# Performance work log

Measured on AMD Instinct MI355X. Metric: run time of the kernel, lower is better.

Reference implementation:

```python
import jax, jax.numpy as jnp
import numpy as np

NA, NM, NT = 4353, 3676, 8000
N = NA + NM + NT
E = 500000
S = 200000
D_IN, DP, DE, DC, HID = 512, 256, 128, 64, 16


def setup_inputs() -> dict:
    key = jax.random.key(0)
    ks = jax.random.split(key, 32)
    f = lambda k, shp, s: (jax.random.normal(k, shp, jnp.float32) * s)
    inp = {
        'h_author': f(ks[0], (NA, D_IN), 1.0),
        'h_movie': f(ks[1], (NM, D_IN), 1.0),
        'h_term': f(ks[2], (NT, D_IN), 1.0),
        'Wp_author': f(ks[3], (D_IN, DP), D_IN ** -0.5),
        'Wp_movie': f(ks[4], (D_IN, DP), D_IN ** -0.5),
        'Wp_term': f(ks[5], (D_IN, DP), D_IN ** -0.5),
        'W1': f(ks[6], (DP, DE), DP ** -0.5),
        'b1': jnp.zeros((DE,), jnp.float32),
        'W2': f(ks[7], (DE, DE), DE ** -0.5),
        'b2': jnp.zeros((DE,), jnp.float32),
        'Wc_author': f(ks[8], (DE, DC), DE ** -0.5),
        'Wc_movie': f(ks[9], (DE, DC), DE ** -0.5),
        'Wc_term': f(ks[10], (DE, DC), DE ** -0.5),
        'Wh_author': f(ks[11], (DE + 2 * DC, HID), (DE + 2 * DC) ** -0.5),
        'Wh_movie': f(ks[12], (DE + 2 * DC, HID), (DE + 2 * DC) ** -0.5),
        'Wh_term': f(ks[13], (DE + 2 * DC, HID), (DE + 2 * DC) ** -0.5),
        'Wo_author': f(ks[14], (HID, 1), HID ** -0.5),
        'Wo_movie': f(ks[15], (HID, 1), HID ** -0.5),
        'Wo_term': f(ks[16], (HID, 1), HID ** -0.5),
        'src': jax.random.randint(ks[17], (E,), 0, N),
        'dst': jax.random.randint(ks[18], (E,), 0, N),
        'ns0_author': jax.random.randint(ks[19], (S,), 0, NA),
        'ns0_movie': jax.random.randint(ks[20], (S,), 0, NM),
        'ns0_term': jax.random.randint(ks[21], (S,), 0, NT),
        'ns1_author': jax.random.randint(ks[22], (S,), 0, NA),
        'ns1_movie': jax.random.randint(ks[23], (S,), 0, NM),
        'ns1_term': jax.random.randint(ks[24], (S,), 0, NT),
        'ns2_author': jax.random.randint(ks[25], (S,), 0, NA),
        'ns2_movie': jax.random.randint(ks[26], (S,), 0, NM),
        'ns2_term': jax.random.randint(ks[27], (S,), 0, NT),
    }
    return inp


def reference(h_author, h_movie, h_term, Wp_author, Wp_movie, Wp_term,
              W1, b1, W2, b2, Wc_author, Wc_movie, Wc_term,
              Wh_author, Wh_movie, Wh_term, Wo_author, Wo_movie, Wo_term,
              src, dst, ns0_author, ns0_movie, ns0_term,
              ns1_author, ns1_movie, ns1_term, ns2_author, ns2_movie, ns2_term):
    # per-ntype feature projection (bias=False), concat in ntype order -> homogeneous [N, DP]
    H = jnp.concatenate([h_author @ Wp_author, h_movie @ Wp_movie, h_term @ Wp_term], axis=0)
    # GraphConv(norm='none'): out = (sum over in-edges of src feat) @ W + b
    agg1 = jax.ops.segment_sum(H[src], dst, num_segments=N)      # [N, DP]
    h1 = jax.nn.relu(agg1 @ W1 + b1)                             # [N, DE]
    agg2 = jax.ops.segment_sum(h1[src], dst, num_segments=N)    # [N, DE]
    h2 = agg2 @ W2 + b2
    # F.normalize(p=2, dim=1, eps=1e-12)
    h = h2 / jnp.maximum(jnp.linalg.norm(h2, axis=1, keepdims=True), 1e-12)
    ha, hm, ht = h[:NA], h[NA:NA + NM], h[NA + NM:]
    # per-ntype context encoder (bias=False)
    ca, cm, ct = ha @ Wc_author, hm @ Wc_movie, ht @ Wc_term

    def cls(feat, Wh, Wo):
        return jax.nn.relu(feat @ Wh) @ Wo  # multi_2Linear, bias=False

    # target emb first, then context of other ntypes in ntype order
    t0 = jnp.concatenate([ha[ns0_author], cm[ns0_movie], ct[ns0_term]], axis=1)
    t1 = jnp.concatenate([hm[ns1_movie], ca[ns1_author], ct[ns1_term]], axis=1)
    t2 = jnp.concatenate([ht[ns2_term], ca[ns2_author], cm[ns2_movie]], axis=1)
    p = jnp.concatenate([cls(t0, Wh_author, Wo_author),
                         cls(t1, Wh_movie, Wo_movie),
                         cls(t2, Wh_term, Wo_term)], axis=0)
    x = jax.nn.sigmoid(p).ravel()
    out_h_movie = h[4353:8029]
    return h, x, out_h_movie
```

## Files before the change

kernel.cpp:

```cpp
#include <hip/hip_runtime.h>
#include <hip/hip_bf16.h>

namespace {
constexpr int kNA = 4353, kNM = 3676, kNT = 8000;
constexpr int kN  = kNA + kNM + kNT;
constexpr int kE  = 500000;
constexpr int kS  = 200000;
constexpr int kDIN = 512, kDP = 256, kDE = 128, kDC = 64;

constexpr size_t OUT_X  = (size_t)kN * kDE;
constexpr size_t OUT_HM = OUT_X + 3ull * kS;

constexpr size_t align256(size_t x) { return (x + 255) & ~size_t(255); }

constexpr size_t OFF_WPW1 = 0;
constexpr size_t OFF_M9   = OFF_WPW1 + 3ull * 512 * 128 * 4;
constexpr size_t OFF_HW1  = align256(OFF_M9 + 9ull * 2048 * 4);
constexpr size_t OFF_H1   = OFF_HW1 + (size_t)kN * kDE * 4;
constexpr size_t OFF_AGG2 = OFF_H1  + (size_t)kN * kDE * 4;
constexpr size_t OFF_HN   = OFF_AGG2 + (size_t)kN * kDE * 4;
constexpr size_t OFF_P    = OFF_HN  + (size_t)kN * kDE * 4;
constexpr size_t OFF_ESRC = align256(OFF_P + 3ull * kN * 16 * 4);
constexpr size_t OFF_RP   = align256(OFF_ESRC + (size_t)kE * 4);
constexpr size_t OFF_CUR  = align256(OFF_RP + (size_t)(kN + 1) * 4);
constexpr size_t WS_NEEDED = align256(OFF_CUR + (size_t)kN * 4);

constexpr int kBA = (kNA + 15) / 16;
constexpr int kBM = (kNM + 15) / 16;
constexpr int kBT = (kNT + 15) / 16;
constexpr int kHW1Blocks = kBA + kBM + kBT;
constexpr int kG2Blocks  = (kN + 15) / 16;
}

__global__ __launch_bounds__(128) void prep1_kernel(
    const float* __restrict__ WpA, const float* __restrict__ WpM,
    const float* __restrict__ WpT, const float* __restrict__ W1,
    float* __restrict__ WpW1)
{
    int b = blockIdx.x;
    int t = b >> 7;
    int k0 = (b & 127) * 4;
    const float* Wp = (t == 0) ? WpA : ((t == 1) ? WpM : WpT);
    int c = threadIdx.x;
    float acc[4] = {0.f, 0.f, 0.f, 0.f};
    for (int j = 0; j < kDP; j++) {
        float w1 = W1[j * kDE + c];
#pragma unroll
        for (int r = 0; r < 4; r++)
            acc[r] += Wp[(k0 + r) * kDP + j] * w1;
    }
#pragma unroll
    for (int r = 0; r < 4; r++)
        WpW1[((size_t)t * kDIN + k0 + r) * kDE + c] = acc[r];
}

__global__ __launch_bounds__(256) void prep2_kernel(
    const float* __restrict__ WhA, const float* __restrict__ WhM,
    const float* __restrict__ WhT,
    const float* __restrict__ WcA, const float* __restrict__ WcM,
    const float* __restrict__ WcT,
    float* __restrict__ M9)
{
    int b = blockIdx.x;
    int g = b / 3, t = b % 3;
    const float* Wh = (g == 0) ? WhA : ((g == 1) ? WhM : WhT);
    const float* Wc = (t == 0) ? WcA : ((t == 1) ? WcM : WcT);
    int slot;
    if (t == g) slot = 0;
    else {
        int lower = (g == 0) ? 1 : 0;
        slot = (t == lower) ? 128 : 192;
    }
    float* Mout = M9 + (size_t)b * 2048;
    for (int idx = threadIdx.x; idx < 2048; idx += 256) {
        int k = idx >> 4, j = idx & 15;
        float v;
        if (slot == 0) v = Wh[k * 16 + j];
        else {
            v = 0.f;
            for (int d = 0; d < kDC; d++)
                v += Wc[k * kDC + d] * Wh[(slot + d) * 16 + j];
        }
        Mout[idx] = v;
    }
}

__global__ __launch_bounds__(256) void hw1_kernel(
    const float* __restrict__ hA, const float* __restrict__ hM,
    const float* __restrict__ hT, const float* __restrict__ WpW1,
    float* __restrict__ HW1)
{
    __shared__ float AL[16 * kDIN];
    int b = blockIdx.x;
    const float *A, *W; int typeN, rowBase, lb;
    if (b < kBA)             { lb = b;             A = hA; W = WpW1;                   typeN = kNA; rowBase = 0; }
    else if (b < kBA + kBM)  { lb = b - kBA;       A = hM; W = WpW1 + 1ull*kDIN*kDE;   typeN = kNM; rowBase = kNA; }
    else                     { lb = b - kBA - kBM; A = hT; W = WpW1 + 2ull*kDIN*kDE;   typeN = kNT; rowBase = kNA + kNM; }
    int r0 = lb * 16;

    const float4* Ag = (const float4*)A;
#pragma unroll
    for (int i = 0; i < 8; i++) {
        int f = threadIdx.x + i * 256;
        int rl = f >> 7, k4 = f & 127;
        int gr = min(r0 + rl, typeN - 1);
        ((float4*)AL)[f] = Ag[(size_t)gr * 128 + k4];
    }
    __syncthreads();

    int col = threadIdx.x & 127;
    int hh  = threadIdx.x >> 7;
    const float* ALh = AL + hh * 8 * kDIN;
    float acc[8];
#pragma unroll
    for (int r = 0; r < 8; r++) acc[r] = 0.f;

    for (int k0 = 0; k0 < kDIN; k0 += 8) {
        float w[8];
#pragma unroll
        for (int i = 0; i < 8; i++)
            w[i] = W[(size_t)(k0 + i) * kDE + col];
#pragma unroll
        for (int r = 0; r < 8; r++) {
            const float4 a0 = *(const float4*)(ALh + r * kDIN + k0);
            const float4 a1 = *(const float4*)(ALh + r * kDIN + k0 + 4);
            acc[r] += a0.x * w[0] + a0.y * w[1] + a0.z * w[2] + a0.w * w[3]
                    + a1.x * w[4] + a1.y * w[5] + a1.z * w[6] + a1.w * w[7];
        }
    }
#pragma unroll
    for (int r = 0; r < 8; r++) {
        int lr = r0 + hh * 8 + r;
        if (lr < typeN) HW1[(size_t)(rowBase + lr) * kDE + col] = acc[r];
    }
}

__device__ __forceinline__ int clampN(int v) { return min(max(v, 0), kN - 1); }

__global__ __launch_bounds__(256) void hist_kernel(const int* __restrict__ key,
                                                   int* __restrict__ counts)
{
    int e = blockIdx.x * 256 + threadIdx.x;
    if (e < kE) atomicAdd(&counts[clampN(key[e])], 1);
}

__global__ __launch_bounds__(256) void scan_kernel(int* __restrict__ cnt_cur,
                                                   int* __restrict__ rowptr)
{
    __shared__ int sums[256];
    int tid = threadIdx.x;
    int i0 = tid * 63, i1 = min(i0 + 63, kN);
    int s = 0;
    for (int i = i0; i < i1; i++) s += cnt_cur[i];
    sums[tid] = s;
    __syncthreads();
    if (tid == 0) {
        int run = 0;
        for (int i = 0; i < 256; i++) { int v = sums[i]; sums[i] = run; run += v; }
    }
    __syncthreads();
    int base = sums[tid];
    for (int i = i0; i < i1; i++) {
        int c = cnt_cur[i];
        rowptr[i] = base;
        cnt_cur[i] = base;
        base += c;
    }
    if (tid == 0) rowptr[kN] = kE;
}

__global__ __launch_bounds__(256) void fill_kernel(const int* __restrict__ stored,
                                                   const int* __restrict__ key,
                                                   int* __restrict__ cursor,
                                                   int* __restrict__ esrc)
{
    int e = blockIdx.x * 256 + threadIdx.x;
    if (e < kE) {
        int p = atomicAdd(&cursor[clampN(key[e])], 1);
        esrc[min(p, kE - 1)] = clampN(stored[e]);
    }
}

__global__ __launch_bounds__(kDE) void agg_relu_kernel(const float* __restrict__ X,
                                                       const int* __restrict__ rowptr,
                                                       const int* __restrict__ esrc,
                                                       const float* __restrict__ b1,
                                                       float* __restrict__ out)
{
    int n = blockIdx.x, tid = threadIdx.x;
    int j = rowptr[n], end = rowptr[n + 1];
    float a0 = 0.f, a1 = 0.f, a2 = 0.f, a3 = 0.f;
    for (; j + 3 < end; j += 4) {
        int s0 = esrc[j], s1 = esrc[j + 1], s2 = esrc[j + 2], s3 = esrc[j + 3];
        a0 += X[(size_t)s0 * kDE + tid];
        a1 += X[(size_t)s1 * kDE + tid];
        a2 += X[(size_t)s2 * kDE + tid];
        a3 += X[(size_t)s3 * kDE + tid];
    }
    for (; j < end; j++) a0 += X[(size_t)esrc[j] * kDE + tid];
    out[(size_t)n * kDE + tid] = fmaxf((a0 + a1) + (a2 + a3) + b1[tid], 0.f);
}

__global__ __launch_bounds__(kDE) void agg_kernel(const float* __restrict__ X,
                                                  const int* __restrict__ rowptr,
                                                  const int* __restrict__ esrc,
                                                  float* __restrict__ out)
{
    int n = blockIdx.x, tid = threadIdx.x;
    int j = rowptr[n], end = rowptr[n + 1];
    float a0 = 0.f, a1 = 0.f, a2 = 0.f, a3 = 0.f;
    for (; j + 3 < end; j += 4) {
        int s0 = esrc[j], s1 = esrc[j + 1], s2 = esrc[j + 2], s3 = esrc[j + 3];
        a0 += X[(size_t)s0 * kDE + tid];
        a1 += X[(size_t)s1 * kDE + tid];
        a2 += X[(size_t)s2 * kDE + tid];
        a3 += X[(size_t)s3 * kDE + tid];
    }
    for (; j < end; j++) a0 += X[(size_t)esrc[j] * kDE + tid];
    out[(size_t)n * kDE + tid] = (a0 + a1) + (a2 + a3);
}

__global__ __launch_bounds__(256) void gemm2_norm_kernel(
    const float* __restrict__ X, const float* __restrict__ W2,
    const float* __restrict__ b2, float* __restrict__ hn,
    float* __restrict__ out)
{
    __shared__ float AL[16 * kDE];
    __shared__ float red[16][2];
    int r0 = blockIdx.x * 16;

    const float4* Xg = (const float4*)X;
#pragma unroll
    for (int i = 0; i < 2; i++) {
        int f = threadIdx.x + i * 256;
        int rl = f >> 5, k4 = f & 31;
        int gr = min(r0 + rl, kN - 1);
        ((float4*)AL)[f] = Xg[(size_t)gr * 32 + k4];
    }
    __syncthreads();

    int col = threadIdx.x & 127;
    int hh  = threadIdx.x >> 7;
    const float* ALh = AL + hh * 8 * kDE;
    float acc[8];
#pragma unroll
    for (int r = 0; r < 8; r++) acc[r] = 0.f;

    for (int k0 = 0; k0 < kDE; k0 += 8) {
        float w[8];
#pragma unroll
        for (int i = 0; i < 8; i++)
            w[i] = W2[(size_t)(k0 + i) * kDE + col];
#pragma unroll
        for (int r = 0; r < 8; r++) {
            const float4 a0 = *(const float4*)(ALh + r * kDE + k0);
            const float4 a1 = *(const float4*)(ALh + r * kDE + k0 + 4);
            acc[r] += a0.x * w[0] + a0.y * w[1] + a0.z * w[2] + a0.w * w[3]
                    + a1.x * w[4] + a1.y * w[5] + a1.z * w[6] + a1.w * w[7];
        }
    }

    float bv = b2[col];
    int half = (threadIdx.x >> 6) & 1;
#pragma unroll
    for (int r = 0; r < 8; r++) {
        float v = acc[r] + bv;
        acc[r] = v;
        float ss = v * v;
#pragma unroll
        for (int o = 32; o > 0; o >>= 1) ss += __shfl_xor(ss, o);
        if ((threadIdx.x & 63) == 0) red[hh * 8 + r][half] = ss;
    }
    __syncthreads();
#pragma unroll
    for (int r = 0; r < 8; r++) {
        int gr = r0 + hh * 8 + r;
        if (gr < kN) {
            float tot = red[hh * 8 + r][0] + red[hh * 8 + r][1];
            float sc = 1.f / fmaxf(sqrtf(tot), 1e-12f);
            float hv = acc[r] * sc;
            hn[(size_t)gr * kDE + col] = hv;
            out[(size_t)gr * kDE + col] = hv;
            if (gr >= kNA && gr < kNA + kNM)
                out[OUT_HM + (size_t)(gr - kNA) * kDE + col] = hv;
        }
    }
}

__global__ __launch_bounds__(128) void partial_kernel(const float* __restrict__ hn,
                                                      const float* __restrict__ M9,
                                                      float* __restrict__ P)
{
    int b = blockIdx.x;
    int g = b / 2005, b2 = b % 2005;
    int t, lb, typeN, rowBase;
    if (b2 < 545)       { t = 0; lb = b2;        typeN = kNA; rowBase = 0; }
    else if (b2 < 1005) { t = 1; lb = b2 - 545;  typeN = kNM; rowBase = kNA; }
    else                { t = 2; lb = b2 - 1005; typeN = kNT; rowBase = kNA + kNM; }
    const float* M = M9 + (size_t)(g * 3 + t) * 2048;
    int r = threadIdx.x >> 4, j = threadIdx.x & 15;
    int lr = lb * 8 + r;
    if (lr >= typeN) return;
    int n = rowBase + lr;
    float acc = 0.f;
    for (int k = 0; k < kDE; k += 4) {
        const float4 h4 = *(const float4*)(hn + (size_t)n * kDE + k);
        acc += h4.x * M[(k + 0) * 16 + j] + h4.y * M[(k + 1) * 16 + j]
             + h4.z * M[(k + 2) * 16 + j] + h4.w * M[(k + 3) * 16 + j];
    }
    P[((size_t)g * kN + n) * 16 + j] = acc;
}

__global__ __launch_bounds__(256) void cls_lite_kernel(
    const float* __restrict__ P,
    const int* __restrict__ n0a, const int* __restrict__ n0m, const int* __restrict__ n0t,
    const int* __restrict__ n1a, const int* __restrict__ n1m, const int* __restrict__ n1t,
    const int* __restrict__ n2a, const int* __restrict__ n2m, const int* __restrict__ n2t,
    const float* __restrict__ WoA, const float* __restrict__ WoM, const float* __restrict__ WoT,
    float* __restrict__ out, int blocksPerGroup)
{
    int g = blockIdx.x / blocksPerGroup;
    int i = (blockIdx.x % blocksPerGroup) * 256 + threadIdx.x;
    if (i >= kS) return;
    auto cA = [](int v){ return min(max(v, 0), kNA - 1); };
    auto cM = [](int v){ return min(max(v, 0), kNM - 1); };
    auto cT = [](int v){ return min(max(v, 0), kNT - 1); };
    int ra, rb, rc;
    if (g == 0)      { ra = cA(n0a[i]);             rb = kNA + cM(n0m[i]);  rc = kNA + kNM + cT(n0t[i]); }
    else if (g == 1) { ra = kNA + cM(n1m[i]);       rb = cA(n1a[i]);        rc = kNA + kNM + cT(n1t[i]); }
    else             { ra = kNA + kNM + cT(n2t[i]); rb = cA(n2a[i]);        rc = kNA + cM(n2m[i]); }
    const float* Pg = P + (size_t)g * kN * 16;
    const float* wo = (g == 0) ? WoA : ((g == 1) ? WoM : WoT);
    const float4* pa = (const float4*)(Pg + (size_t)ra * 16);
    const float4* pb = (const float4*)(Pg + (size_t)rb * 16);
    const float4* pc = (const float4*)(Pg + (size_t)rc * 16);
    float p = 0.f;
#pragma unroll
    for (int q = 0; q < 4; q++) {
        float4 a = pa[q], b = pb[q], c = pc[q];
        p += fmaxf(a.x + b.x + c.x, 0.f) * wo[q * 4 + 0];
        p += fmaxf(a.y + b.y + c.y, 0.f) * wo[q * 4 + 1];
        p += fmaxf(a.z + b.z + c.z, 0.f) * wo[q * 4 + 2];
        p += fmaxf(a.w + b.w + c.w, 0.f) * wo[q * 4 + 3];
    }
    out[OUT_X + (size_t)g * kS + i] = 1.f / (1.f + expf(-p));
}

extern "C" void kernel_launch(void* const* d_in, const int* in_sizes, int n_in,
                              void* d_out, int out_size, void* d_ws, size_t ws_size,
                              hipStream_t stream)
{
    (void)out_size;
    static const int expected[30] = {
        2228736, 1882112, 4096000, 131072, 131072, 131072, 32768, 128, 16384, 128,
        8192, 8192, 8192, 4096, 4096, 4096, 16, 16, 16,
        500000, 500000, 200000, 200000, 200000, 200000, 200000, 200000, 200000, 200000, 200000 };
    if (n_in != 30) return;
    for (int i = 0; i < 30; i++) if (in_sizes[i] != expected[i]) return;
    if (ws_size < WS_NEEDED) return;

    const float* h_a  = (const float*)d_in[0];
    const float* h_m  = (const float*)d_in[1];
    const float* h_t  = (const float*)d_in[2];
    const float* Wp_a = (const float*)d_in[3];
    const float* Wp_m = (const float*)d_in[4];
    const float* Wp_t = (const float*)d_in[5];
    const float* W1   = (const float*)d_in[6];
    const float* b1   = (const float*)d_in[7];
    const float* W2   = (const float*)d_in[8];
    const float* b2   = (const float*)d_in[9];
    const float* Wc_a = (const float*)d_in[10];
    const float* Wc_m = (const float*)d_in[11];
    const float* Wc_t = (const float*)d_in[12];
    const float* Wh_a = (const float*)d_in[13];
    const float* Wh_m = (const float*)d_in[14];
    const float* Wh_t = (const float*)d_in[15];
    const float* Wo_a = (const float*)d_in[16];
    const float* Wo_m = (const float*)d_in[17];
    const float* Wo_t = (const float*)d_in[18];
    const int* src = (const int*)d_in[19];
    const int* dst = (const int*)d_in[20];

    char* ws = (char*)d_ws;
    float* WpW1  = (float*)(ws + OFF_WPW1);
    float* M9    = (float*)(ws + OFF_M9);
    float* HW1   = (float*)(ws + OFF_HW1);
    float* h1    = (float*)(ws + OFF_H1);
    float* agg2  = (float*)(ws + OFF_AGG2);
    float* hn    = (float*)(ws + OFF_HN);
    float* P     = (float*)(ws + OFF_P);
    int* esrc    = (int*)(ws + OFF_ESRC);
    int* rowptr  = (int*)(ws + OFF_RP);
    int* cursor  = (int*)(ws + OFF_CUR);
    float* out   = (float*)d_out;

    hipMemsetAsync(cursor, 0, (size_t)kN * 4, stream);

    hist_kernel<<<dim3(1954), dim3(256), 0, stream>>>(dst, cursor);
    scan_kernel<<<dim3(1), dim3(256), 0, stream>>>(cursor, rowptr);
    fill_kernel<<<dim3(1954), dim3(256), 0, stream>>>(src, dst, cursor, esrc);

    prep1_kernel<<<dim3(384), dim3(128), 0, stream>>>(Wp_a, Wp_m, Wp_t, W1, WpW1);
    prep2_kernel<<<dim3(9), dim3(256), 0, stream>>>(Wh_a, Wh_m, Wh_t, Wc_a, Wc_m, Wc_t, M9);

    hw1_kernel<<<dim3(kHW1Blocks), dim3(256), 0, stream>>>(h_a, h_m, h_t, WpW1, HW1);
    agg_relu_kernel<<<dim3(kN), dim3(kDE), 0, stream>>>(HW1, rowptr, esrc, b1, h1);
    agg_kernel<<<dim3(kN), dim3(kDE), 0, stream>>>(h1, rowptr, esrc, agg2);
    gemm2_norm_kernel<<<dim3(kG2Blocks), dim3(256), 0, stream>>>(agg2, W2, b2, hn, out);
    partial_kernel<<<dim3(6015), dim3(128), 0, stream>>>(hn, M9, P);
    cls_lite_kernel<<<dim3(2346), dim3(256), 0, stream>>>(P,
        (const int*)d_in[21], (const int*)d_in[22], (const int*)d_in[23],
        (const int*)d_in[24], (const int*)d_in[25], (const int*)d_in[26],
        (const int*)d_in[27], (const int*)d_in[28], (const int*)d_in[29],
        Wo_a, Wo_m, Wo_t, out, 782);
}
```

Baseline: 296.7 us.

## Register-tile hw1 GEMM with float4 and parallelize edge aggregation across warps

```diff
diff --git a/kernel.cpp b/kernel.cpp
--- a/kernel.cpp
+++ b/kernel.cpp
@@ -30,6 +30,7 @@
 constexpr int kBT = (kNT + 15) / 16;
 constexpr int kHW1Blocks = kBA + kBM + kBT;
 constexpr int kG2Blocks  = (kN + 15) / 16;
+constexpr int kAPad = kDIN + 4;
 }
 
 __global__ __launch_bounds__(128) void prep1_kernel(
@@ -90,7 +91,7 @@
     const float* __restrict__ hT, const float* __restrict__ WpW1,
     float* __restrict__ HW1)
 {
-    __shared__ float AL[16 * kDIN];
+    __shared__ float AL[16 * kAPad];
     int b = blockIdx.x;
     const float *A, *W; int typeN, rowBase, lb;
     if (b < kBA)             { lb = b;             A = hA; W = WpW1;                   typeN = kNA; rowBase = 0; }
@@ -104,35 +105,43 @@
         int f = threadIdx.x + i * 256;
         int rl = f >> 7, k4 = f & 127;
         int gr = min(r0 + rl, typeN - 1);
-        ((float4*)AL)[f] = Ag[(size_t)gr * 128 + k4];
-    }
-    __syncthreads();
-
-    int col = threadIdx.x & 127;
-    int hh  = threadIdx.x >> 7;
-    const float* ALh = AL + hh * 8 * kDIN;
-    float acc[8];
-#pragma unroll
-    for (int r = 0; r < 8; r++) acc[r] = 0.f;
-
-    for (int k0 = 0; k0 < kDIN; k0 += 8) {
-        float w[8];
-#pragma unroll
-        for (int i = 0; i < 8; i++)
-            w[i] = W[(size_t)(k0 + i) * kDE + col];
-#pragma unroll
-        for (int r = 0; r < 8; r++) {
-            const float4 a0 = *(const float4*)(ALh + r * kDIN + k0);
-            const float4 a1 = *(const float4*)(ALh + r * kDIN + k0 + 4);
-            acc[r] += a0.x * w[0] + a0.y * w[1] + a0.z * w[2] + a0.w * w[3]
-                    + a1.x * w[4] + a1.y * w[5] + a1.z * w[6] + a1.w * w[7];
-        }
-    }
-#pragma unroll
-    for (int r = 0; r < 8; r++) {
-        int lr = r0 + hh * 8 + r;
-        if (lr < typeN) HW1[(size_t)(rowBase + lr) * kDE + col] = acc[r];
-    }
+        *(float4*)(AL + rl * kAPad + k4 * 4) = Ag[(size_t)gr * 128 + k4];
+    }
+    __syncthreads();
+
+    int wave = threadIdx.x >> 6, lane = threadIdx.x & 63;
+    int cg = wave * 8 + (lane & 7);
+    int rg = lane >> 3;
+    int colbase = cg * 4;
+    const float* AL0 = AL + (2 * rg) * kAPad;
+    const float* AL1 = AL + (2 * rg + 1) * kAPad;
+
+    float4 acc0 = {0.f, 0.f, 0.f, 0.f};
+    float4 acc1 = {0.f, 0.f, 0.f, 0.f};
+
+#pragma unroll 2
+    for (int k0 = 0; k0 < kDIN; k0 += 4) {
+        const float4 w0 = *(const float4*)(W + (size_t)(k0 + 0) * kDE + colbase);
+        const float4 w1 = *(const float4*)(W + (size_t)(k0 + 1) * kDE + colbase);
+        const float4 w2 = *(const float4*)(W + (size_t)(k0 + 2) * kDE + colbase);
+        const float4 w3 = *(const float4*)(W + (size_t)(k0 + 3) * kDE + colbase);
+        const float4 a0 = *(const float4*)(AL0 + k0);
+        const float4 a1 = *(const float4*)(AL1 + k0);
+        acc0.x += a0.x * w0.x + a0.y * w1.x + a0.z * w2.x + a0.w * w3.x;
+        acc0.y += a0.x * w0.y + a0.y * w1.y + a0.z * w2.y + a0.w * w3.y;
+        acc0.z += a0.x * w0.z + a0.y * w1.z + a0.z * w2.z + a0.w * w3.z;
+        acc0.w += a0.x * w0.w + a0.y * w1.w + a0.z * w2.w + a0.w * w3.w;
+        acc1.x += a1.x * w0.x + a1.y * w1.x + a1.z * w2.x + a1.w * w3.x;
+        acc1.y += a1.x * w0.y + a1.y * w1.y + a1.z * w2.y + a1.w * w3.y;
+        acc1.z += a1.x * w0.z + a1.y * w1.z + a1.z * w2.z + a1.w * w3.z;
+        acc1.w += a1.x * w0.w + a1.y * w1.w + a1.z * w2.w + a1.w * w3.w;
+    }
+
+    int lr0 = r0 + 2 * rg, lr1 = lr0 + 1;
+    if (lr0 < typeN)
+        *(float4*)(HW1 + (size_t)(rowBase + lr0) * kDE + colbase) = acc0;
+    if (lr1 < typeN)
+        *(float4*)(HW1 + (size_t)(rowBase + lr1) * kDE + colbase) = acc1;
 }
 
 __device__ __forceinline__ int clampN(int v) { return min(max(v, 0), kN - 1); }
@@ -181,43 +190,45 @@
     }
 }
 
-__global__ __launch_bounds__(kDE) void agg_relu_kernel(const float* __restrict__ X,
-                                                       const int* __restrict__ rowptr,
-                                                       const int* __restrict__ esrc,
-                                                       const float* __restrict__ b1,
-                                                       float* __restrict__ out)
-{
-    int n = blockIdx.x, tid = threadIdx.x;
-    int j = rowptr[n], end = rowptr[n + 1];
-    float a0 = 0.f, a1 = 0.f, a2 = 0.f, a3 = 0.f;
-    for (; j + 3 < end; j += 4) {
-        int s0 = esrc[j], s1 = esrc[j + 1], s2 = esrc[j + 2], s3 = esrc[j + 3];
-        a0 += X[(size_t)s0 * kDE + tid];
-        a1 += X[(size_t)s1 * kDE + tid];
-        a2 += X[(size_t)s2 * kDE + tid];
-        a3 += X[(size_t)s3 * kDE + tid];
-    }
-    for (; j < end; j++) a0 += X[(size_t)esrc[j] * kDE + tid];
-    out[(size_t)n * kDE + tid] = fmaxf((a0 + a1) + (a2 + a3) + b1[tid], 0.f);
-}
-
-__global__ __launch_bounds__(kDE) void agg_kernel(const float* __restrict__ X,
-                                                  const int* __restrict__ rowptr,
-                                                  const int* __restrict__ esrc,
-                                                  float* __restrict__ out)
-{
-    int n = blockIdx.x, tid = threadIdx.x;
-    int j = rowptr[n], end = rowptr[n + 1];
-    float a0 = 0.f, a1 = 0.f, a2 = 0.f, a3 = 0.f;
-    for (; j + 3 < end; j += 4) {
-        int s0 = esrc[j], s1 = esrc[j + 1], s2 = esrc[j + 2], s3 = esrc[j + 3];
-        a0 += X[(size_t)s0 * kDE + tid];
-        a1 += X[(size_t)s1 * kDE + tid];
-        a2 += X[(size_t)s2 * kDE + tid];
-        a3 += X[(size_t)s3 * kDE + tid];
-    }
-    for (; j < end; j++) a0 += X[(size_t)esrc[j] * kDE + tid];
-    out[(size_t)n * kDE + tid] = (a0 + a1) + (a2 + a3);
+template <bool RELU>
+__global__ __launch_bounds__(256) void agg4_kernel(const float* __restrict__ X,
+                                                   const int* __restrict__ rowptr,
+                                                   const int* __restrict__ esrc,
+                                                   const float* __restrict__ b1,
+                                                   float* __restrict__ out)
+{
+    __shared__ float4 sh[8][32];
+    int n = blockIdx.x;
+    int eo = threadIdx.x >> 5;
+    int cg = threadIdx.x & 31;
+    int start = rowptr[n], end = rowptr[n + 1];
+    const float4* X4 = (const float4*)X;
+    float4 acc = {0.f, 0.f, 0.f, 0.f};
+    for (int j = start + eo; j < end; j += 8) {
+        int s = esrc[j];
+        float4 v = X4[(size_t)s * 32 + cg];
+        acc.x += v.x; acc.y += v.y; acc.z += v.z; acc.w += v.w;
+    }
+    sh[eo][cg] = acc;
+    __syncthreads();
+    if (threadIdx.x < 32) {
+        int c = threadIdx.x;
+        float4 s0 = sh[0][c], s1 = sh[1][c], s2 = sh[2][c], s3 = sh[3][c];
+        float4 s4 = sh[4][c], s5 = sh[5][c], s6 = sh[6][c], s7 = sh[7][c];
+        float4 r;
+        r.x = ((s0.x + s1.x) + (s2.x + s3.x)) + ((s4.x + s5.x) + (s6.x + s7.x));
+        r.y = ((s0.y + s1.y) + (s2.y + s3.y)) + ((s4.y + s5.y) + (s6.y + s7.y));
+        r.z = ((s0.z + s1.z) + (s2.z + s3.z)) + ((s4.z + s5.z) + (s6.z + s7.z));
+        r.w = ((s0.w + s1.w) + (s2.w + s3.w)) + ((s4.w + s5.w) + (s6.w + s7.w));
+        if (RELU) {
+            const float4 bv = ((const float4*)b1)[c];
+            r.x = fmaxf(r.x + bv.x, 0.f);
+            r.y = fmaxf(r.y + bv.y, 0.f);
+            r.z = fmaxf(r.z + bv.z, 0.f);
+            r.w = fmaxf(r.w + bv.w, 0.f);
+        }
+        ((float4*)out)[(size_t)n * 32 + c] = r;
+    }
 }
 
 __global__ __launch_bounds__(256) void gemm2_norm_kernel(
@@ -404,8 +415,8 @@
     prep2_kernel<<<dim3(9), dim3(256), 0, stream>>>(Wh_a, Wh_m, Wh_t, Wc_a, Wc_m, Wc_t, M9);
 
     hw1_kernel<<<dim3(kHW1Blocks), dim3(256), 0, stream>>>(h_a, h_m, h_t, WpW1, HW1);
-    agg_relu_kernel<<<dim3(kN), dim3(kDE), 0, stream>>>(HW1, rowptr, esrc, b1, h1);
-    agg_kernel<<<dim3(kN), dim3(kDE), 0, stream>>>(h1, rowptr, esrc, agg2);
+    agg4_kernel<true><<<dim3(kN), dim3(256), 0, stream>>>(HW1, rowptr, esrc, b1, h1);
+    agg4_kernel<false><<<dim3(kN), dim3(256), 0, stream>>>(h1, rowptr, esrc, b1, agg2);
     gemm2_norm_kernel<<<dim3(kG2Blocks), dim3(256), 0, stream>>>(agg2, W2, b2, hn, out);
     partial_kernel<<<dim3(6015), dim3(128), 0, stream>>>(hn, M9, P);
     cls_lite_kernel<<<dim3(2346), dim3(256), 0, stream>>>(P,
```

New measurement: 316.0 us. 1.07x slower.
